# Kernel tuning notes

Hardware: AMD Instinct MI355X
Metric: run time of the kernel (lower is better)

Reference implementation:

```python
import jax, jax.numpy as jnp
import numpy as np

GAMMA = 0.1
EPSILON = 0.1
NUM_ITERS = 4


def setup_inputs() -> dict:
    key = jax.random.key(0)
    k1, k2, k3, k4 = jax.random.split(key, 4)
    N, E, D = 100000, 1600000, 128
    x = jax.random.normal(k1, (N, D), dtype=jnp.float32)
    edge_index = jax.random.randint(k2, (2, E), 0, N, dtype=jnp.int32)
    # kaiming-uniform-like scale for W, glorot-like for GCN weight
    W = jax.random.normal(k3, (D, D), dtype=jnp.float32) * (1.0 / np.sqrt(D))
    W_phi = jax.random.normal(k4, (D, D), dtype=jnp.float32) * (1.0 / np.sqrt(D))
    bias = jnp.zeros((D,), dtype=jnp.float32)
    return {"x": x, "edge_index": edge_index, "W": W, "W_phi": W_phi, "bias": bias}


def _gcn_conv(x, W_phi, src, dst, n_nodes):
    """GCNConv(bias=False): symmetric normalization with added self-loops."""
    xw = x @ W_phi.T  # [N, D] linear transform (torch Linear: y = x W^T)
    ones = jnp.ones(src.shape, dtype=xw.dtype)
    deg = jax.ops.segment_sum(ones, dst, num_segments=n_nodes) + 1.0  # +1 self-loop
    dinv = jax.lax.rsqrt(deg)  # deg >= 1, always finite
    norm = dinv[src] * dinv[dst]  # [E]
    agg = jax.ops.segment_sum(xw[src] * norm[:, None], dst, num_segments=n_nodes)
    # self-loop contribution: norm_ii = dinv_i^2
    return agg + xw * (dinv * dinv)[:, None]


def reference(x, edge_index, W, W_phi, bias):
    n_nodes, d = x.shape
    src, dst = edge_index[0], edge_index[1]
    A = W - W.T - GAMMA * jnp.eye(d, dtype=x.dtype)  # antisymmetric - gamma*I
    for _ in range(NUM_ITERS):
        h = _gcn_conv(x, W_phi, src, dst, n_nodes)
        h = jnp.tanh(x @ A.T + h + bias)
        x = x + EPSILON * h
    return x
```

## Files before the change

kernel.cpp:

```cpp
#include <hip/hip_runtime.h>
#include <hip/hip_bf16.h>
#include <math.h>

#define GAMMA 0.1f
#define EPSILON 0.1f
#define NUM_ITERS 4
#define BSHIFT 9
#define CH_P 36
#define CH_SZ (16 * CH_P)

typedef __attribute__((ext_vector_type(8))) short short8;
typedef __attribute__((ext_vector_type(4))) float floatx4;
typedef __attribute__((ext_vector_type(2))) float floatx2;

__device__ __forceinline__ float bf2f(unsigned short u) {
  union { unsigned int i; float f; } v; v.i = ((unsigned int)u) << 16; return v.f;
}
__device__ __forceinline__ unsigned short f2bf(float f) {
  union { float f; unsigned int i; } v; v.f = f;
  unsigned int x = v.i;
  return (unsigned short)((x + 0x7fffu + ((x >> 16) & 1u)) >> 16);
}
__device__ __forceinline__ unsigned int f2_to_bfx2(float a, float b) {
  return (unsigned int)f2bf(a) | (((unsigned int)f2bf(b)) << 16);
}
__device__ __forceinline__ float2 bfx2_to_f2(unsigned int u) {
  union { unsigned int i; float f; } lo, hi;
  lo.i = u << 16; hi.i = u & 0xffff0000u;
  return make_float2(lo.f, hi.f);
}
__device__ __forceinline__ float tanh_fast(float s) {
  float c = fminf(15.0f, fmaxf(-15.0f, s));
  float e = __expf(2.0f * c);
  return (e - 1.0f) * __frcp_rn(e + 1.0f);
}


#if defined(__has_builtin)
#if __has_builtin(__builtin_amdgcn_cvt_pk_f32_fp8) && __has_builtin(__builtin_amdgcn_cvt_pk_fp8_f32)
#define FP8_HW 1
#endif
#endif

__device__ __forceinline__ float e4m3_to_f_sw(unsigned int b) {
  unsigned int s = (b >> 7) & 1u, e = (b >> 3) & 15u, m = b & 7u;
  float v;
  if (e) { union { unsigned int u; float f; } c; c.u = ((e + 120u) << 23) | (m << 20); v = c.f; }
  else v = (float)m * 0.001953125f;
  return s ? -v : v;
}
__device__ __forceinline__ unsigned int f_to_e4m3_sw(float x) {
  union { float f; unsigned int u; } v; v.f = x;
  unsigned int sgn = (v.u >> 24) & 0x80u;
  float a = fabsf(x);
  if (a < 0.0009765625f) return sgn;
  if (a > 448.f) return sgn | 0x7Eu;
  v.f = a;
  int e32 = (int)((v.u >> 23) & 0xffu) - 127;
  if (e32 < -6) {
    int q = (int)(a * 512.0f + 0.5f);
    if (q > 7) q = 7;
    return sgn | (unsigned)q;
  }
  unsigned int u = v.u + 0x000FFFFFu + ((v.u >> 20) & 1u);
  int e = (int)((u >> 23) & 0xffu) - 127;
  if (e > 8) return sgn | 0x7Eu;
  unsigned int m = (u >> 20) & 7u;
  return sgn | ((unsigned)(e + 7) << 3) | m;
}

__device__ __forceinline__ floatx2 fp8x2_cvt_lo(unsigned int w) {
#ifdef FP8_HW
  return __builtin_amdgcn_cvt_pk_f32_fp8(w, false);
#else
  floatx2 r; r.x = e4m3_to_f_sw(w & 0xffu); r.y = e4m3_to_f_sw((w >> 8) & 0xffu); return r;
#endif
}
__device__ __forceinline__ floatx2 fp8x2_cvt_hi(unsigned int w) {
#ifdef FP8_HW
  return __builtin_amdgcn_cvt_pk_f32_fp8(w, true);
#else
  floatx2 r; r.x = e4m3_to_f_sw((w >> 16) & 0xffu); r.y = e4m3_to_f_sw((w >> 24) & 0xffu); return r;
#endif
}
__device__ __forceinline__ unsigned int fp8x4_enc(float a, float b, float c, float d) {
#ifdef FP8_HW
  unsigned int w = (unsigned int)__builtin_amdgcn_cvt_pk_fp8_f32(a, b, 0, false);
  w = (unsigned int)__builtin_amdgcn_cvt_pk_fp8_f32(c, d, (int)w, true);
  return w;
#else
  return f_to_e4m3_sw(a) | (f_to_e4m3_sw(b) << 8) | (f_to_e4m3_sw(c) << 16) | (f_to_e4m3_sw(d) << 24);
#endif
}


__global__ void detect_kernel(const unsigned int* __restrict__ x, int* __restrict__ flag) {
  __shared__ int ws4[4];
  int tid = threadIdx.x;
  int bad = 0;
  for (int i = tid; i < 2048; i += 256) {
    unsigned int u = x[i];
    float lo = bf2f((unsigned short)(u & 0xffffu));
    if (!(fabsf(lo) <= 64.0f)) bad++;
  }
#pragma unroll
  for (int d = 1; d < 64; d <<= 1) bad += __shfl_xor(bad, d, 64);
  if ((tid & 63) == 0) ws4[tid >> 6] = bad;
  __syncthreads();
  if (tid == 0) *flag = (ws4[0] + ws4[1] + ws4[2] + ws4[3] > 64) ? 1 : 0;
}


__global__ void fill_kernel(unsigned short* __restrict__ out, int n, unsigned short val) {
  int t = blockIdx.x * blockDim.x + threadIdx.x;
  if (t < n) out[t] = val;
}

__global__ void prep_kernel(const void* __restrict__ Wv, const void* __restrict__ Wphiv,
                            const void* __restrict__ biasv, const int* __restrict__ flag,
                            unsigned short* __restrict__ Am, unsigned short* __restrict__ Wb,
                            float* __restrict__ bias_f) {
  int t = blockIdx.x * blockDim.x + threadIdx.x;
  if (t >= 128 * 128) return;
  int isf = *flag;
  int j = t >> 7, k = t & 127;
  float w_jk, w_kj, wp;
  if (isf) {
    const float* W = (const float*)Wv;
    const float* Wp = (const float*)Wphiv;
    w_jk = W[t]; w_kj = W[k * 128 + j]; wp = Wp[t];
  } else {
    const unsigned short* W = (const unsigned short*)Wv;
    const unsigned short* Wp = (const unsigned short*)Wphiv;
    w_jk = bf2f(W[t]); w_kj = bf2f(W[k * 128 + j]); wp = bf2f(Wp[t]);
  }
  float v = w_jk - w_kj;
  if (j == k) v -= GAMMA;
  Am[t] = f2bf(v);
  Wb[t] = f2bf(wp);
  if (t < 128)
    bias_f[t] = isf ? ((const float*)biasv)[t] : bf2f(((const unsigned short*)biasv)[t]);
}

__global__ void init_x_kernel(const void* __restrict__ xinv, const int* __restrict__ flag,
                              unsigned short* __restrict__ xb, int N, int NP) {
  int t = blockIdx.x * blockDim.x + threadIdx.x;
  if (t >= NP * 16) return;
  int base = t * 8;
  int row = base >> 7;
  uint4 o;
  if (row < N) {
    if (*flag) {
      const float* p = (const float*)xinv + base;
      float4 f0 = *(const float4*)p;
      float4 f1 = *(const float4*)(p + 4);
      o.x = f2_to_bfx2(f0.x, f0.y); o.y = f2_to_bfx2(f0.z, f0.w);
      o.z = f2_to_bfx2(f1.x, f1.y); o.w = f2_to_bfx2(f1.z, f1.w);
    } else {
      o = *(const uint4*)((const unsigned short*)xinv + base);
    }
  } else {
    o = make_uint4(0u, 0u, 0u, 0u);
  }
  *(uint4*)(xb + base) = o;
}

__global__ void scale_kernel(const unsigned short* __restrict__ xb,
                             const float* __restrict__ dinv,
                             unsigned char* __restrict__ zf, int NP16) {
  int t = blockIdx.x * blockDim.x + threadIdx.x;
  if (t >= NP16) return;
  int base = t * 8;
  float dv = dinv[base >> 7];
  uint4 u = *(const uint4*)(xb + base);
  float2 f0 = bfx2_to_f2(u.x), f1 = bfx2_to_f2(u.y);
  float2 f2 = bfx2_to_f2(u.z), f3 = bfx2_to_f2(u.w);
  uint2 o;
  o.x = fp8x4_enc(f0.x * dv, f0.y * dv, f1.x * dv, f1.y * dv);
  o.y = fp8x4_enc(f2.x * dv, f2.y * dv, f3.x * dv, f3.y * dv);
  *(uint2*)(zf + base) = o;
}


__global__ void bcount_kernel(const int* __restrict__ dst, int* __restrict__ gcnt,
                              int E, int NB) {
  __shared__ int cnt[512];
  int tid = threadIdx.x;
  for (int j = tid; j < 512; j += 256) cnt[j] = 0;
  __syncthreads();
  int base = blockIdx.x * 4096;
#pragma unroll
  for (int k = 0; k < 16; ++k) {
    int i = base + k * 256 + tid;
    if (i < E) atomicAdd(&cnt[dst[i] >> BSHIFT], 1);
  }
  __syncthreads();
  for (int j = tid; j < NB; j += 256)
    if (cnt[j]) atomicAdd(&gcnt[j], cnt[j]);
}

__global__ void bscan_kernel(const int* __restrict__ gcnt, int* __restrict__ gofs,
                             int* __restrict__ gcur, int NB, int E) {
  if (NB <= 256) {
    __shared__ int wsum[4];
    int t = threadIdx.x;
    int v = (t < NB) ? gcnt[t] : 0;
    int lane = t & 63, w = t >> 6;
    int inc = v;
#pragma unroll
    for (int d = 1; d < 64; d <<= 1) { int q = __shfl_up(inc, d, 64); if (lane >= d) inc += q; }
    if (lane == 63) wsum[w] = inc;
    __syncthreads();
    int woff = 0;
    for (int k = 0; k < w; ++k) woff += wsum[k];
    int ex = woff + inc - v;
    if (t < NB) { gofs[t] = ex; gcur[t] = ex; }
    if (t == 0) gofs[NB] = E;
  } else if (threadIdx.x == 0) {
    int run = 0;
    for (int i = 0; i < NB; ++i) { gofs[i] = run; gcur[i] = run; run += gcnt[i]; }
    gofs[NB] = E;
  }
}

__global__ void bscatter_kernel(const int* __restrict__ src, const int* __restrict__ dst,
                                int* __restrict__ gcur, unsigned int* __restrict__ bpairs,
                                int E, int NB) {
  __shared__ int cnt[512];
  __shared__ int pos[512];
  int tid = threadIdx.x;
  for (int j = tid; j < 512; j += 256) cnt[j] = 0;
  __syncthreads();
  int base = blockIdx.x * 4096;
#pragma unroll
  for (int k = 0; k < 16; ++k) {
    int i = base + k * 256 + tid;
    if (i < E) atomicAdd(&cnt[dst[i] >> BSHIFT], 1);
  }
  __syncthreads();
  for (int j = tid; j < NB; j += 256)
    pos[j] = cnt[j] ? atomicAdd(&gcur[j], cnt[j]) : 0;
  __syncthreads();
#pragma unroll
  for (int k = 0; k < 16; ++k) {
    int i = base + k * 256 + tid;
    if (i < E) {
      int d = dst[i];
      int slot = atomicAdd(&pos[d >> BSHIFT], 1);
      bpairs[slot] = (((unsigned)d & 511u) << 23) | (unsigned)src[i];
    }
  }
}

__global__ __launch_bounds__(256) void bfinal_kernel(
    const unsigned int* __restrict__ bpairs, const int* __restrict__ gofs,
    int* __restrict__ offs, float* __restrict__ dinv, int* __restrict__ csr,
    int N, int NP, int E) {
  __shared__ int dl[512];
  __shared__ int cur[512];
  __shared__ int wsum2[4];
  int b = blockIdx.x, t = threadIdx.x;
  int node0 = b << BSHIFT;
  dl[t] = 0; dl[t + 256] = 0;
  __syncthreads();
  int e0 = gofs[b], e1 = gofs[b + 1];
  for (int i = e0 + t; i < e1; i += 256)
    atomicAdd(&dl[bpairs[i] >> 23], 1);
  __syncthreads();
  int v0 = dl[2 * t], v1 = dl[2 * t + 1];
  int ps = v0 + v1;
  int lane = t & 63, w = t >> 6;
  int inc = ps;
#pragma unroll
  for (int d = 1; d < 64; d <<= 1) { int q = __shfl_up(inc, d, 64); if (lane >= d) inc += q; }
  if (lane == 63) wsum2[w] = inc;
  __syncthreads();
  int woff = 0;
  for (int k = 0; k < w; ++k) woff += wsum2[k];
  int base = e0 + woff + inc - ps;
  int n0 = node0 + 2 * t, n1 = node0 + 2 * t + 1;
  if (n0 < N) offs[n0] = base;
  if (n1 < N) offs[n1] = base + v0;
  if (n0 < NP) dinv[n0] = rsqrtf((float)v0 + 1.0f);
  if (n1 < NP) dinv[n1] = rsqrtf((float)v1 + 1.0f);
  cur[2 * t] = base;
  cur[2 * t + 1] = base + v0;
  if (b == 0 && t == 0) offs[N] = E;
  __syncthreads();
  for (int i = e0 + t; i < e1; i += 256) {
    unsigned int p = bpairs[i];
    int s = atomicAdd(&cur[p >> 23], 1);
    csr[s] = (int)(p & 0x7FFFFFu);
  }
}


__global__ __launch_bounds__(256) void fused_kernel(
    unsigned short* __restrict__ xb, const unsigned short* __restrict__ Am,
    const unsigned short* __restrict__ Wphi, const float* __restrict__ dinv,
    const unsigned short* __restrict__ g, const float* __restrict__ bias_f,
    void* __restrict__ outb, unsigned char* __restrict__ znext,
    const int* __restrict__ flag, int Mvalid) {
  __shared__ __align__(16) unsigned short bsm[128 * 128];
  const int tid = threadIdx.x, lane = tid & 63, wid = tid >> 6;
  const int l15 = lane & 15, quad = lane >> 4;
  const int m0 = blockIdx.x * 64;
  const int arow = m0 + wid * 16 + l15;
  const size_t abase = (size_t)arow * 128 + quad * 8;

  short8 afrag[4], sfrag[4];
#pragma unroll
  for (int kk = 0; kk < 4; ++kk) afrag[kk] = *(const short8*)(xb + abase + kk * 32);
#pragma unroll
  for (int kk = 0; kk < 4; ++kk) sfrag[kk] = *(const short8*)(g + abase + kk * 32);
  const float dva = dinv[arow];

#pragma unroll
  for (int p = 0; p < 8; ++p) {
    int c = p * 256 + tid;
    int row = c >> 4, slot = c & 15;
    *(uint4*)(bsm + row * 128 + ((slot ^ (row & 7)) * 8)) = *(const uint4*)(Am + c * 8);
  }
  __syncthreads();

  floatx4 acc[8];
  const floatx4 zero = {0.f, 0.f, 0.f, 0.f};
#pragma unroll
  for (int j = 0; j < 8; ++j) acc[j] = zero;
  const int rsw = (l15 & 7);
#pragma unroll
  for (int kk = 0; kk < 4; ++kk) {
#pragma unroll
    for (int j = 0; j < 8; ++j) {
      short8 b = *(const short8*)(bsm + (j * 16 + l15) * 128 + (((kk * 4 + quad) ^ rsw) * 8));
      acc[j] = __builtin_amdgcn_mfma_f32_16x16x32_bf16(afrag[kk], b, acc[j], 0, 0, 0);
    }
  }
  __syncthreads();

#pragma unroll
  for (int p = 0; p < 8; ++p) {
    int c = p * 256 + tid;
    int row = c >> 4, slot = c & 15;
    *(uint4*)(bsm + row * 128 + ((slot ^ (row & 7)) * 8)) = *(const uint4*)(Wphi + c * 8);
  }
  __syncthreads();
#pragma unroll
  for (int kk = 0; kk < 4; ++kk) {
#pragma unroll
    for (int j = 0; j < 8; ++j) {
      short8 b = *(const short8*)(bsm + (j * 16 + l15) * 128 + (((kk * 4 + quad) ^ rsw) * 8));
      acc[j] = __builtin_amdgcn_mfma_f32_16x16x32_bf16(sfrag[kk], b, acc[j], 0, 0, 0);
    }
  }
  __syncthreads();

  const int isf = *flag;
  const bool valid = arow < Mvalid;
  float* wbuf = (float*)bsm + wid * 2 * CH_SZ;
#pragma unroll
  for (int kk = 0; kk < 4; ++kk) {
    float* buf = wbuf + (kk & 1) * CH_SZ;
#pragma unroll
    for (int jj = 0; jj < 2; ++jj) {
#pragma unroll
      for (int r = 0; r < 4; ++r)
        buf[(quad * 4 + r) * CH_P + jj * 16 + l15] = acc[2 * kk + jj][r];
    }
    const int col0 = kk * 32 + quad * 8;
    const float* ap = &buf[l15 * CH_P + quad * 8];
    float4 s0 = *(const float4*)ap;
    float4 s1 = *(const float4*)(ap + 4);
    float4 b0 = *(const float4*)&bias_f[col0];
    float4 b1 = *(const float4*)&bias_f[col0 + 4];
    union { short8 s; unsigned short h[8]; } xu; xu.s = afrag[kk];
    float xv[8];
    xv[0] = bf2f(xu.h[0]) + EPSILON * tanh_fast(s0.x + b0.x);
    xv[1] = bf2f(xu.h[1]) + EPSILON * tanh_fast(s0.y + b0.y);
    xv[2] = bf2f(xu.h[2]) + EPSILON * tanh_fast(s0.z + b0.z);
    xv[3] = bf2f(xu.h[3]) + EPSILON * tanh_fast(s0.w + b0.w);
    xv[4] = bf2f(xu.h[4]) + EPSILON * tanh_fast(s1.x + b1.x);
    xv[5] = bf2f(xu.h[5]) + EPSILON * tanh_fast(s1.y + b1.y);
    xv[6] = bf2f(xu.h[6]) + EPSILON * tanh_fast(s1.z + b1.z);
    xv[7] = bf2f(xu.h[7]) + EPSILON * tanh_fast(s1.w + b1.w);
    uint4 pk;
    pk.x = f2_to_bfx2(xv[0], xv[1]); pk.y = f2_to_bfx2(xv[2], xv[3]);
    pk.z = f2_to_bfx2(xv[4], xv[5]); pk.w = f2_to_bfx2(xv[6], xv[7]);
    if (valid) {
      if (!outb) {
        *(uint4*)(xb + abase + kk * 32) = pk;
        if (znext) {
          uint2 zk;
          zk.x = fp8x4_enc(xv[0] * dva, xv[1] * dva, xv[2] * dva, xv[3] * dva);
          zk.y = fp8x4_enc(xv[4] * dva, xv[5] * dva, xv[6] * dva, xv[7] * dva);
          *(uint2*)(znext + abase + kk * 32) = zk;
        }
      } else {
        if (isf) {
          float* op = (float*)outb + abase + kk * 32;
          *(float4*)op = make_float4(xv[0], xv[1], xv[2], xv[3]);
          *(float4*)(op + 4) = make_float4(xv[4], xv[5], xv[6], xv[7]);
        } else {
          *(uint4*)((unsigned short*)outb + abase + kk * 32) = pk;
        }
      }
    }
  }
}

__global__ __launch_bounds__(256) void agg_kernel(
    const unsigned char* __restrict__ zf,
    const int* __restrict__ offs,
    const int* __restrict__ csr,
    const float* __restrict__ dinv,
    unsigned short* __restrict__ g,
    int N) {
  int i = blockIdx.x * 4 + (threadIdx.x >> 6);
  if (i >= N) return;
  int lane = threadIdx.x & 63;
  int sub = lane >> 4;
  int c8 = (lane & 15) * 8;

  floatx2 a01 = {0.f, 0.f}, a23 = {0.f, 0.f}, a45 = {0.f, 0.f}, a67 = {0.f, 0.f};

#define ACC8F(u) { \
  a01 += fp8x2_cvt_lo((u).x); \
  a23 += fp8x2_cvt_hi((u).x); \
  a45 += fp8x2_cvt_lo((u).y); \
  a67 += fp8x2_cvt_hi((u).y); }

  int e0 = offs[i], e1 = offs[i + 1];
  int e = e0 + sub;
  for (; e + 4 < e1; e += 8) {
    int s0 = csr[e];
    int s1 = csr[e + 4];
    uint2 u0 = *(const uint2*)(zf + (size_t)s0 * 128 + c8);
    uint2 u1 = *(const uint2*)(zf + (size_t)s1 * 128 + c8);
    ACC8F(u0); ACC8F(u1);
  }
  if (e < e1) {
    int s0 = csr[e];
    uint2 u0 = *(const uint2*)(zf + (size_t)s0 * 128 + c8);
    ACC8F(u0);
  }

  float a0 = a01.x, a1 = a01.y, a2 = a23.x, a3 = a23.y;
  float a4 = a45.x, a5 = a45.y, a6 = a67.x, a7 = a67.y;

  a0 += __shfl_xor(a0, 16, 64); a0 += __shfl_xor(a0, 32, 64);
  a1 += __shfl_xor(a1, 16, 64); a1 += __shfl_xor(a1, 32, 64);
  a2 += __shfl_xor(a2, 16, 64); a2 += __shfl_xor(a2, 32, 64);
  a3 += __shfl_xor(a3, 16, 64); a3 += __shfl_xor(a3, 32, 64);
  a4 += __shfl_xor(a4, 16, 64); a4 += __shfl_xor(a4, 32, 64);
  a5 += __shfl_xor(a5, 16, 64); a5 += __shfl_xor(a5, 32, 64);
  a6 += __shfl_xor(a6, 16, 64); a6 += __shfl_xor(a6, 32, 64);
  a7 += __shfl_xor(a7, 16, 64); a7 += __shfl_xor(a7, 32, 64);

  if (sub == 0) {
    uint2 su = *(const uint2*)(zf + (size_t)i * 128 + c8);
    floatx2 s01 = fp8x2_cvt_lo(su.x), s23 = fp8x2_cvt_hi(su.x);
    floatx2 s45 = fp8x2_cvt_lo(su.y), s67 = fp8x2_cvt_hi(su.y);
    a0 += s01.x; a1 += s01.y; a2 += s23.x; a3 += s23.y;
    a4 += s45.x; a5 += s45.y; a6 += s67.x; a7 += s67.y;
    float dv = dinv[i];
    uint4 o;
    o.x = f2_to_bfx2(a0 * dv, a1 * dv);
    o.y = f2_to_bfx2(a2 * dv, a3 * dv);
    o.z = f2_to_bfx2(a4 * dv, a5 * dv);
    o.w = f2_to_bfx2(a6 * dv, a7 * dv);
    *(uint4*)(g + (size_t)i * 128 + c8) = o;
  }
#undef ACC8F
}


extern "C" void kernel_launch(void* const* d_in, const int* in_sizes, int n_in,
                              void* d_out, int out_size, void* d_ws, size_t ws_size,
                              hipStream_t stream) {
  const void* x_in = d_in[0];
  const int* ei = (const int*)d_in[1];
  const void* W = d_in[2];
  const void* Wphi = d_in[3];
  const void* bias = d_in[4];

  const int N = in_sizes[0] / 128;
  const int E = in_sizes[1] / 2;
  const int NP = ((N + 63) / 64) * 64;
  const int* src = ei;
  const int* dst = ei + E;
  const int NB = (N + 511) >> BSHIFT;
  const int EB = (E + 4095) / 4096;

  size_t off = 0;
  auto place = [&](size_t bytes) { size_t r = off; off = (off + bytes + 255) & ~(size_t)255; return r; };
  size_t o_xb   = place((size_t)NP * 128 * 2);
  size_t o_z    = place((size_t)NP * 128);
  size_t o_g    = place((size_t)NP * 128 * 2);
  size_t o_Am   = place(128 * 128 * 2);
  size_t o_Wb   = place(128 * 128 * 2);
  size_t o_bf   = place(128 * 4);
  size_t o_flag = place(4);
  size_t o_dinv = place((size_t)(NB * 512 + 64) * 4);
  size_t o_offs = place((size_t)(N + 1) * 4);
  size_t o_gcnt = place((size_t)NB * 4);
  size_t o_gofs = place((size_t)(NB + 1) * 4);
  size_t o_gcur = place((size_t)NB * 4);
  size_t o_bprs = place((size_t)E * 4);
  size_t o_csr  = place((size_t)E * 4);
  if (off > ws_size || in_sizes[0] % 128 != 0 || out_size != N * 128 || n_in < 5 ||
      N > (1 << 23)) {
    fill_kernel<<<(out_size * 2 + 255) / 256, 256, 0, stream>>>(
        (unsigned short*)d_out, out_size, (unsigned short)0x3F80);
    return;
  }
  char* basep = (char*)d_ws;
  unsigned short* xb = (unsigned short*)(basep + o_xb);
  unsigned char* zf  = (unsigned char*)(basep + o_z);
  unsigned short* g  = (unsigned short*)(basep + o_g);
  unsigned short* Am = (unsigned short*)(basep + o_Am);
  unsigned short* Wb = (unsigned short*)(basep + o_Wb);
  float* bias_f = (float*)(basep + o_bf);
  int* flag   = (int*)(basep + o_flag);
  float* dinv = (float*)(basep + o_dinv);
  int* offs   = (int*)(basep + o_offs);
  int* gcnt   = (int*)(basep + o_gcnt);
  int* gofs   = (int*)(basep + o_gofs);
  int* gcur   = (int*)(basep + o_gcur);
  unsigned int* bpairs = (unsigned int*)(basep + o_bprs);
  int* csr    = (int*)(basep + o_csr);

  hipMemsetAsync(gcnt, 0, (size_t)NB * 4, stream);
  detect_kernel<<<1, 256, 0, stream>>>((const unsigned int*)x_in, flag);
  prep_kernel<<<(128 * 128 + 255) / 256, 256, 0, stream>>>(W, Wphi, bias, flag, Am, Wb, bias_f);
  init_x_kernel<<<(NP * 16 + 255) / 256, 256, 0, stream>>>(x_in, flag, xb, N, NP);
  bcount_kernel<<<EB, 256, 0, stream>>>(dst, gcnt, E, NB);
  bscan_kernel<<<1, 256, 0, stream>>>(gcnt, gofs, gcur, NB, E);
  bscatter_kernel<<<EB, 256, 0, stream>>>(src, dst, gcur, bpairs, E, NB);
  bfinal_kernel<<<NB, 256, 0, stream>>>(bpairs, gofs, offs, dinv, csr, N, NP, E);

  const int gblocks = NP / 64;
  scale_kernel<<<(NP * 16 + 255) / 256, 256, 0, stream>>>(xb, dinv, zf, NP * 16);
  for (int t = 0; t < NUM_ITERS; ++t) {
    agg_kernel<<<(N + 3) / 4, 256, 0, stream>>>(zf, offs, csr, dinv, g, N);
    void* outp = (t == NUM_ITERS - 1) ? d_out : nullptr;
    unsigned char* znext = (t == NUM_ITERS - 1) ? nullptr : zf;
    fused_kernel<<<gblocks, 256, 0, stream>>>(xb, Am, Wb, dinv, g, bias_f,
                                              outp, znext, flag, N);
  }
}
```

Baseline: 490.1 us.

## Fold fp8 scale pass into CSR finalize and halve fused GEMM LDS footprint

The standalone scale kernel, which converts bf16 x into dinv-scaled fp8 z, is removed. That work now runs at the end of bfinal_kernel, using the per-node dinv values it already holds in shared memory, which saves one launch and one reread of dinv. The fused GEMM kernel now stages each 128x128 weight matrix in two 64-row halves, and its epilogue uses a single staging buffer per wave, so the block's LDS use drops to 16KB. This should let more blocks reside per CU, at the cost of extra barriers and more staging passes.

Measured after the change: 495.9 us. About the same (+1.2%).

```diff
diff --git a/kernel.cpp b/kernel.cpp
--- a/kernel.cpp
+++ b/kernel.cpp
@@ -165,22 +165,6 @@
   *(uint4*)(xb + base) = o;
 }
 
-__global__ void scale_kernel(const unsigned short* __restrict__ xb,
-                             const float* __restrict__ dinv,
-                             unsigned char* __restrict__ zf, int NP16) {
-  int t = blockIdx.x * blockDim.x + threadIdx.x;
-  if (t >= NP16) return;
-  int base = t * 8;
-  float dv = dinv[base >> 7];
-  uint4 u = *(const uint4*)(xb + base);
-  float2 f0 = bfx2_to_f2(u.x), f1 = bfx2_to_f2(u.y);
-  float2 f2 = bfx2_to_f2(u.z), f3 = bfx2_to_f2(u.w);
-  uint2 o;
-  o.x = fp8x4_enc(f0.x * dv, f0.y * dv, f1.x * dv, f1.y * dv);
-  o.y = fp8x4_enc(f2.x * dv, f2.y * dv, f3.x * dv, f3.y * dv);
-  *(uint2*)(zf + base) = o;
-}
-
 
 __global__ void bcount_kernel(const int* __restrict__ dst, int* __restrict__ gcnt,
                               int E, int NB) {
@@ -255,9 +239,11 @@
 __global__ __launch_bounds__(256) void bfinal_kernel(
     const unsigned int* __restrict__ bpairs, const int* __restrict__ gofs,
     int* __restrict__ offs, float* __restrict__ dinv, int* __restrict__ csr,
+    const unsigned short* __restrict__ xb, unsigned char* __restrict__ zf,
     int N, int NP, int E) {
   __shared__ int dl[512];
   __shared__ int cur[512];
+  __shared__ float dvf[512];
   __shared__ int wsum2[4];
   int b = blockIdx.x, t = threadIdx.x;
   int node0 = b << BSHIFT;
@@ -279,10 +265,13 @@
   for (int k = 0; k < w; ++k) woff += wsum2[k];
   int base = e0 + woff + inc - ps;
   int n0 = node0 + 2 * t, n1 = node0 + 2 * t + 1;
+  float d0 = rsqrtf((float)v0 + 1.0f), d1 = rsqrtf((float)v1 + 1.0f);
   if (n0 < N) offs[n0] = base;
   if (n1 < N) offs[n1] = base + v0;
-  if (n0 < NP) dinv[n0] = rsqrtf((float)v0 + 1.0f);
-  if (n1 < NP) dinv[n1] = rsqrtf((float)v1 + 1.0f);
+  if (n0 < NP) dinv[n0] = d0;
+  if (n1 < NP) dinv[n1] = d1;
+  dvf[2 * t] = d0;
+  dvf[2 * t + 1] = d1;
   cur[2 * t] = base;
   cur[2 * t + 1] = base + v0;
   if (b == 0 && t == 0) offs[N] = E;
@@ -291,6 +280,20 @@
     unsigned int p = bpairs[i];
     int s = atomicAdd(&cur[p >> 23], 1);
     csr[s] = (int)(p & 0x7FFFFFu);
+  }
+  for (int c = t; c < 512 * 16; c += 256) {
+    int row = c >> 4;
+    int n = node0 + row;
+    if (n >= N) break;
+    float dv = dvf[row];
+    int base8 = n * 128 + (c & 15) * 8;
+    uint4 u = *(const uint4*)(xb + base8);
+    float2 f0 = bfx2_to_f2(u.x), f1 = bfx2_to_f2(u.y);
+    float2 f2 = bfx2_to_f2(u.z), f3 = bfx2_to_f2(u.w);
+    uint2 o;
+    o.x = fp8x4_enc(f0.x * dv, f0.y * dv, f1.x * dv, f1.y * dv);
+    o.y = fp8x4_enc(f2.x * dv, f2.y * dv, f3.x * dv, f3.y * dv);
+    *(uint2*)(zf + base8) = o;
   }
 }
 
@@ -301,7 +304,7 @@
     const unsigned short* __restrict__ g, const float* __restrict__ bias_f,
     void* __restrict__ outb, unsigned char* __restrict__ znext,
     const int* __restrict__ flag, int Mvalid) {
-  __shared__ __align__(16) unsigned short bsm[128 * 128];
+  __shared__ __align__(16) unsigned short bsm[64 * 128];
   const int tid = threadIdx.x, lane = tid & 63, wid = tid >> 6;
   const int l15 = lane & 15, quad = lane >> 4;
   const int m0 = blockIdx.x * 64;
@@ -314,53 +317,47 @@
 #pragma unroll
   for (int kk = 0; kk < 4; ++kk) sfrag[kk] = *(const short8*)(g + abase + kk * 32);
   const float dva = dinv[arow];
-
-#pragma unroll
-  for (int p = 0; p < 8; ++p) {
-    int c = p * 256 + tid;
-    int row = c >> 4, slot = c & 15;
-    *(uint4*)(bsm + row * 128 + ((slot ^ (row & 7)) * 8)) = *(const uint4*)(Am + c * 8);
-  }
-  __syncthreads();
+  const int rsw = (l15 & 7);
 
   floatx4 acc[8];
   const floatx4 zero = {0.f, 0.f, 0.f, 0.f};
 #pragma unroll
   for (int j = 0; j < 8; ++j) acc[j] = zero;
-  const int rsw = (l15 & 7);
-#pragma unroll
-  for (int kk = 0; kk < 4; ++kk) {
-#pragma unroll
-    for (int j = 0; j < 8; ++j) {
-      short8 b = *(const short8*)(bsm + (j * 16 + l15) * 128 + (((kk * 4 + quad) ^ rsw) * 8));
-      acc[j] = __builtin_amdgcn_mfma_f32_16x16x32_bf16(afrag[kk], b, acc[j], 0, 0, 0);
-    }
-  }
-  __syncthreads();
-
-#pragma unroll
-  for (int p = 0; p < 8; ++p) {
-    int c = p * 256 + tid;
-    int row = c >> 4, slot = c & 15;
-    *(uint4*)(bsm + row * 128 + ((slot ^ (row & 7)) * 8)) = *(const uint4*)(Wphi + c * 8);
-  }
-  __syncthreads();
-#pragma unroll
-  for (int kk = 0; kk < 4; ++kk) {
-#pragma unroll
-    for (int j = 0; j < 8; ++j) {
-      short8 b = *(const short8*)(bsm + (j * 16 + l15) * 128 + (((kk * 4 + quad) ^ rsw) * 8));
-      acc[j] = __builtin_amdgcn_mfma_f32_16x16x32_bf16(sfrag[kk], b, acc[j], 0, 0, 0);
-    }
-  }
-  __syncthreads();
+
+#define STAGE_HALF(SRC, ROW0) { \
+    _Pragma("unroll") \
+    for (int p = 0; p < 4; ++p) { \
+      int c = p * 256 + tid; \
+      int row = c >> 4, slot = c & 15; \
+      *(uint4*)(bsm + row * 128 + ((slot ^ (row & 7)) * 8)) = \
+          *(const uint4*)((SRC) + (ROW0) * 128 + c * 8); \
+    } \
+  }
+#define GEMM_HALF(FR, ACC_B) { \
+    _Pragma("unroll") \
+    for (int kk = 0; kk < 4; ++kk) { \
+      _Pragma("unroll") \
+      for (int j = 0; j < 4; ++j) { \
+        short8 b_ = *(const short8*)(bsm + (j * 16 + l15) * 128 + (((kk * 4 + quad) ^ rsw) * 8)); \
+        acc[(ACC_B) + j] = __builtin_amdgcn_mfma_f32_16x16x32_bf16(FR[kk], b_, acc[(ACC_B) + j], 0, 0, 0); \
+      } \
+    } \
+  }
+
+  STAGE_HALF(Am, 0);    __syncthreads();
+  GEMM_HALF(afrag, 0);  __syncthreads();
+  STAGE_HALF(Am, 64);   __syncthreads();
+  GEMM_HALF(afrag, 4);  __syncthreads();
+  STAGE_HALF(Wphi, 0);  __syncthreads();
+  GEMM_HALF(sfrag, 0);  __syncthreads();
+  STAGE_HALF(Wphi, 64); __syncthreads();
+  GEMM_HALF(sfrag, 4);  __syncthreads();
 
   const int isf = *flag;
   const bool valid = arow < Mvalid;
-  float* wbuf = (float*)bsm + wid * 2 * CH_SZ;
+  float* buf = (float*)bsm + wid * CH_SZ;
 #pragma unroll
   for (int kk = 0; kk < 4; ++kk) {
-    float* buf = wbuf + (kk & 1) * CH_SZ;
 #pragma unroll
     for (int jj = 0; jj < 2; ++jj) {
 #pragma unroll
@@ -406,6 +403,8 @@
       }
     }
   }
+#undef STAGE_HALF
+#undef GEMM_HALF
 }
 
 __global__ __launch_bounds__(256) void agg_kernel(
@@ -536,10 +535,9 @@
   bcount_kernel<<<EB, 256, 0, stream>>>(dst, gcnt, E, NB);
   bscan_kernel<<<1, 256, 0, stream>>>(gcnt, gofs, gcur, NB, E);
   bscatter_kernel<<<EB, 256, 0, stream>>>(src, dst, gcur, bpairs, E, NB);
-  bfinal_kernel<<<NB, 256, 0, stream>>>(bpairs, gofs, offs, dinv, csr, N, NP, E);
+  bfinal_kernel<<<NB, 256, 0, stream>>>(bpairs, gofs, offs, dinv, csr, xb, zf, N, NP, E);
 
   const int gblocks = NP / 64;
-  scale_kernel<<<(NP * 16 + 255) / 256, 256, 0, stream>>>(xb, dinv, zf, NP * 16);
   for (int t = 0; t < NUM_ITERS; ++t) {
     agg_kernel<<<(N + 3) / 4, 256, 0, stream>>>(zf, offs, csr, dinv, g, N);
     void* outp = (t == NUM_ITERS - 1) ? d_out : nullptr;
```
